# Kernel tuning notes

Measured on AMD Instinct MI355X. Metric: run time of the kernel, lower is better.

The kernel has to match this reference:

```python
import jax, jax.numpy as jnp
import numpy as np

LAT_SIZE = 2048
BATCH = 4096


def cos_pos_encoding_1d(size, freq_div=2.0, sub_freq_max=4.0):
    freqs = list(range(1, int(size / freq_div)))
    spaces = [np.linspace(0, freq * 2 * np.pi, size) for freq in freqs]
    sub_freqs = [1.0 / float(i) for i in range(2, int(sub_freq_max))]
    sub_spaces = [np.linspace(i * freq * 2 * np.pi, (i + 1) * freq * 2 * np.pi, size)
                  for freq in sub_freqs for i in range(int(1 / freq))]
    spaces = spaces + sub_spaces
    cos = [np.cos(space) for space in spaces]
    return np.stack(cos).astype(np.float32)  # (n_freq, size)


def setup_inputs() -> dict:
    key = jax.random.key(0)
    k1, k2 = jax.random.split(key)
    cos_basis = jnp.asarray(cos_pos_encoding_1d(LAT_SIZE, 1, 8))  # (2074, 2048)
    n_freq = cos_basis.shape[0]
    x = jax.random.normal(k1, (BATCH, LAT_SIZE), dtype=jnp.float32)
    # nn.Linear default init: U(-1/sqrt(in), 1/sqrt(in))
    bound = 1.0 / np.sqrt(LAT_SIZE)
    W = jax.random.uniform(k2, (n_freq, LAT_SIZE), dtype=jnp.float32,
                           minval=-bound, maxval=bound)
    return {"x": x, "W": W, "cos_basis": cos_basis}


def reference(x, W, cos_basis):
    # x: (B, lat), W: (n_freq, lat), cos_basis: (n_freq, lat)
    x_freqs = x @ W.T                          # (B, n_freq)  -- to_freq_size
    # broadcast-mul + sum over freq dim == GEMM against fixed cosine basis
    out = x_freqs @ cos_basis                  # (B, lat)
    # global max-normalize (norm=True)
    return out / jnp.max(out)
```

## Files before the change

### kernel.cpp

```cpp
#include <hip/hip_runtime.h>
#include <hip/hip_bf16.h>
#include <cstdint>

#define BATCH 4096
#define LAT   2048
#define NFREQ 2074
#define KPAD  2112

typedef __bf16 bf16x8 __attribute__((ext_vector_type(8)));
typedef float  f32x4  __attribute__((ext_vector_type(4)));

__device__ __forceinline__ unsigned short f2bf(float f) {
    unsigned int u = __float_as_uint(f);
    u = (u + 0x7fffu + ((u >> 16) & 1u)) >> 16;
    return (unsigned short)u;
}

__device__ __forceinline__ void gload_lds16(const unsigned short* g, unsigned short* l) {
    __builtin_amdgcn_global_load_lds(
        (const __attribute__((address_space(1))) unsigned int*)g,
        (__attribute__((address_space(3))) unsigned int*)l,
        16, 0, 0);
}


__global__ void prep_kernel(const float* __restrict__ W,
                            const float* __restrict__ cb,
                            unsigned short* __restrict__ WT,
                            unsigned short* __restrict__ cosT,
                            float* __restrict__ maxp) {
    __shared__ float t[64][65];
    const int bid = blockIdx.x;
    const int tid = threadIdx.x;
    if (bid == 0 && tid == 0) *maxp = -__builtin_inff();
    const float* in     = (bid < 1056) ? W  : cb;
    unsigned short* out = (bid < 1056) ? WT : cosT;
    int b2 = (bid < 1056) ? bid : bid - 1056;
    const int c0 = (b2 % 32) * 64;
    const int r0 = (b2 / 32) * 64;
    for (int i = tid; i < 1024; i += 256) {
        int rr = i >> 4;
        int c4 = (i & 15) * 4;
        int r  = r0 + rr;
        float4 v;
        if (r < NFREQ) v = *(const float4*)&in[(size_t)r * LAT + c0 + c4];
        else           v = make_float4(0.f, 0.f, 0.f, 0.f);
        t[rr][c4 + 0] = v.x; t[rr][c4 + 1] = v.y;
        t[rr][c4 + 2] = v.z; t[rr][c4 + 3] = v.w;
    }
    __syncthreads();
    for (int i = tid; i < 1024; i += 256) {
        int cc = i >> 4;
        int r4 = (i & 15) * 4;
        ushort4 o;
        o.x = f2bf(t[r4 + 0][cc]); o.y = f2bf(t[r4 + 1][cc]);
        o.z = f2bf(t[r4 + 2][cc]); o.w = f2bf(t[r4 + 3][cc]);
        *(ushort4*)&out[(size_t)(c0 + cc) * KPAD + r0 + r4] = o;
    }
}

template <int N, int K>
__global__ __launch_bounds__(512, 4)
void gemm1_kernel(const unsigned short* __restrict__ A,
                  const unsigned short* __restrict__ Bt,
                  unsigned short* __restrict__ C,
                  const float* __restrict__ x,
                  unsigned short* __restrict__ xb) {
    if (blockIdx.y >= 16) {
        const int cb  = (blockIdx.y - 16) * 16 + blockIdx.x;
        const int tid = threadIdx.x;
        const float4* x4 = (const float4*)x;
        uint4* o4 = (uint4*)xb;
        int i = cb * 512 + tid;
#pragma unroll
        for (int it = 0; it < 8; ++it, i += 131072) {
            float4 a = x4[2 * i];
            float4 b = x4[2 * i + 1];
            union { unsigned short us[8]; uint4 v; } p;
            p.us[0] = f2bf(a.x); p.us[1] = f2bf(a.y); p.us[2] = f2bf(a.z); p.us[3] = f2bf(a.w);
            p.us[4] = f2bf(b.x); p.us[5] = f2bf(b.y); p.us[6] = f2bf(b.z); p.us[7] = f2bf(b.w);
            o4[i] = p.v;
        }
        return;
    }

    __shared__ alignas(16) unsigned short As[3][128 * 32];
    __shared__ alignas(16) unsigned short Bs[3][128 * 32];

    const int tid  = threadIdx.x;
    const int wave = tid >> 6;
    const int lane = tid & 63;
    const int wm   = (wave >> 2) * 64;
    const int wn   = (wave & 3) * 32;
    const int quad = lane >> 4;
    const int l16  = lane & 15;

    const int mBase = blockIdx.y * 128;
    const int nBase = blockIdx.x * 128;

    const int srow = lane >> 2;
    const int sk   = (((lane & 3) ^ ((srow >> 1) & 3))) * 8;

    const unsigned short* Ab1 = A  + (size_t)(mBase + wave * 16 + srow) * K + sk;
    const unsigned short* Bb1 = Bt + (size_t)(nBase + wave * 16 + srow) * K + sk;
    const int coff = (wave * 16) * 32;

    const int pc = (quad ^ ((l16 >> 1) & 3)) * 8;

    constexpr int NIT = K / 32;
    gload_lds16(Ab1, &As[0][coff]);
    gload_lds16(Bb1, &Bs[0][coff]);

    f32x4 acc[4][2] = {};
    int bc = 0;
    for (int j = 0; j < NIT; ++j) {
        const int bn = (bc == 2) ? 0 : bc + 1;
        if (j + 1 < NIT) {
            const int k0 = (j + 1) * 32;
            gload_lds16(Ab1 + k0, &As[bn][coff]);
            gload_lds16(Bb1 + k0, &Bs[bn][coff]);
            asm volatile("s_waitcnt vmcnt(2)\n\ts_barrier" ::: "memory");
        } else {
            asm volatile("s_waitcnt vmcnt(0)\n\ts_barrier" ::: "memory");
        }
        bf16x8 af[4], bfr[2];
#pragma unroll
        for (int mi = 0; mi < 4; ++mi)
            af[mi] = *(const bf16x8*)&As[bc][(wm + mi * 16 + l16) * 32 + pc];
#pragma unroll
        for (int ni = 0; ni < 2; ++ni)
            bfr[ni] = *(const bf16x8*)&Bs[bc][(wn + ni * 16 + l16) * 32 + pc];
#pragma unroll
        for (int mi = 0; mi < 4; ++mi)
#pragma unroll
            for (int ni = 0; ni < 2; ++ni)
                acc[mi][ni] = __builtin_amdgcn_mfma_f32_16x16x32_bf16(
                    af[mi], bfr[ni], acc[mi][ni], 0, 0, 0);
        bc = bn;
    }

#pragma unroll
    for (int mi = 0; mi < 4; ++mi)
#pragma unroll
        for (int ni = 0; ni < 2; ++ni) {
            int col = nBase + wn + ni * 16 + l16;
#pragma unroll
            for (int r = 0; r < 4; ++r) {
                int row = mBase + wm + mi * 16 + quad * 4 + r;
                C[(size_t)row * N + col] = f2bf(acc[mi][ni][r]);
            }
        }
}

template <int N, int K>
__global__ __launch_bounds__(512, 4)
void gemm2_kernel(const unsigned short* __restrict__ A,
                  const unsigned short* __restrict__ Bt,
                  float* __restrict__ C,
                  float* __restrict__ maxp) {
    __shared__ alignas(16) unsigned short As[3][128 * 32];
    __shared__ alignas(16) unsigned short Bs[3][128 * 32];
    __shared__ float redbuf[8];

    const int tid  = threadIdx.x;
    const int wave = tid >> 6;
    const int lane = tid & 63;
    const int wm   = (wave >> 2) * 64;
    const int wn   = (wave & 3) * 32;
    const int quad = lane >> 4;
    const int l16  = lane & 15;

    const int mBase = blockIdx.y * 128;
    const int nBase = blockIdx.x * 128;

    const int srow = lane >> 2;
    const int sk   = (((lane & 3) ^ ((srow >> 1) & 3))) * 8;

    const unsigned short* Ab1 = A  + (size_t)(mBase + wave * 16 + srow) * K + sk;
    const unsigned short* Bb1 = Bt + (size_t)(nBase + wave * 16 + srow) * K + sk;
    const int coff = (wave * 16) * 32;

    const int pc = (quad ^ ((l16 >> 1) & 3)) * 8;

    constexpr int NIT = K / 32;
    gload_lds16(Ab1, &As[0][coff]);
    gload_lds16(Bb1, &Bs[0][coff]);

    f32x4 acc[4][2] = {};
    int bc = 0;
    for (int j = 0; j < NIT; ++j) {
        const int bn = (bc == 2) ? 0 : bc + 1;
        if (j + 1 < NIT) {
            const int k0 = (j + 1) * 32;
            gload_lds16(Ab1 + k0, &As[bn][coff]);
            gload_lds16(Bb1 + k0, &Bs[bn][coff]);
            asm volatile("s_waitcnt vmcnt(2)\n\ts_barrier" ::: "memory");
        } else {
            asm volatile("s_waitcnt vmcnt(0)\n\ts_barrier" ::: "memory");
        }
        bf16x8 af[4], bfr[2];
#pragma unroll
        for (int mi = 0; mi < 4; ++mi)
            af[mi] = *(const bf16x8*)&As[bc][(wm + mi * 16 + l16) * 32 + pc];
#pragma unroll
        for (int ni = 0; ni < 2; ++ni)
            bfr[ni] = *(const bf16x8*)&Bs[bc][(wn + ni * 16 + l16) * 32 + pc];
#pragma unroll
        for (int mi = 0; mi < 4; ++mi)
#pragma unroll
            for (int ni = 0; ni < 2; ++ni)
                acc[mi][ni] = __builtin_amdgcn_mfma_f32_16x16x32_bf16(
                    af[mi], bfr[ni], acc[mi][ni], 0, 0, 0);
        bc = bn;
    }

    float vmax = -__builtin_inff();
#pragma unroll
    for (int mi = 0; mi < 4; ++mi)
#pragma unroll
        for (int ni = 0; ni < 2; ++ni) {
            int col = nBase + wn + ni * 16 + l16;
#pragma unroll
            for (int r = 0; r < 4; ++r) {
                int row = mBase + wm + mi * 16 + quad * 4 + r;
                float v = acc[mi][ni][r];
                C[(size_t)row * N + col] = v;
                vmax = fmaxf(vmax, v);
            }
        }
#pragma unroll
    for (int off = 32; off > 0; off >>= 1)
        vmax = fmaxf(vmax, __shfl_xor(vmax, off));
    if (lane == 0) redbuf[wave] = vmax;
    __syncthreads();
    if (tid == 0) {
        float m = redbuf[0];
#pragma unroll
        for (int w = 1; w < 8; ++w) m = fmaxf(m, redbuf[w]);
        if (m >= 0.0f) atomicMax((int*)maxp, __float_as_int(m));
        else           atomicMin((unsigned int*)maxp, __float_as_uint(m));
    }
}

__global__ void scale_kernel(float* __restrict__ out, const float* __restrict__ maxp) {
    int i = blockIdx.x * blockDim.x + threadIdx.x;
    float inv = 1.0f / (*maxp);
    float4* o4 = (float4*)out;
    float4 v = o4[i];
    v.x *= inv; v.y *= inv; v.z *= inv; v.w *= inv;
    o4[i] = v;
}

extern "C" void kernel_launch(void* const* d_in, const int* in_sizes, int n_in,
                              void* d_out, int out_size, void* d_ws, size_t ws_size,
                              hipStream_t stream) {
    const float* x  = (const float*)d_in[0];
    const float* W  = (const float*)d_in[1];
    const float* cb = (const float*)d_in[2];

    char* ws = (char*)d_ws;
    unsigned short* xb   = (unsigned short*)ws;
    unsigned short* WT   = (unsigned short*)(ws + (size_t)BATCH * LAT * 2);
    unsigned short* cosT = (unsigned short*)((char*)WT + (size_t)LAT * KPAD * 2);
    unsigned short* C1   = (unsigned short*)((char*)cosT + (size_t)LAT * KPAD * 2);
    float*          maxp = (float*)((char*)C1 + (size_t)LAT * LAT * 2);
    float*          out  = (float*)d_out;

    prep_kernel<<<2 * 1056, 256, 0, stream>>>(W, cb, WT, cosT, maxp);

    gemm1_kernel<LAT, KPAD>
        <<<dim3(16, 32), 512, 0, stream>>>(cosT, WT, C1, x, xb);

    gemm2_kernel<LAT, LAT>
        <<<dim3(LAT / 128, BATCH / 128), 512, 0, stream>>>(xb, C1, out, maxp);

    scale_kernel<<<(out_size / 4) / 256, 256, 0, stream>>>(out, maxp);
}
```

Measured before the change: 191.6 us.

## Store GEMM2 output as bf16 intermediate and widen block to 1024 threads

GEMM2 now writes a bf16 intermediate through nontemporal stores instead of fp32 output, and the scale kernel reads that bf16 buffer and writes the final fp32 normalized result. This cuts the write-then-reread fp32 round trip between GEMM2 and the scale pass. The GEMM2 block goes to 1024 threads (16 waves), each wave holding a 32x32 tile and issuing one LDS load instead of two, to raise wave-level parallelism. GEMM1 output stores also become nontemporal. Rounding the output to bf16 before scaling adds precision loss, and the 1024-thread blocks with (1024,8) launch bounds may constrain registers.

```diff
diff --git a/kernel.cpp b/kernel.cpp
--- a/kernel.cpp
+++ b/kernel.cpp
@@ -147,25 +147,26 @@
 #pragma unroll
             for (int r = 0; r < 4; ++r) {
                 int row = mBase + wm + mi * 16 + quad * 4 + r;
-                C[(size_t)row * N + col] = f2bf(acc[mi][ni][r]);
+                __builtin_nontemporal_store(f2bf(acc[mi][ni][r]),
+                                            &C[(size_t)row * N + col]);
             }
         }
 }
 
 template <int N, int K>
-__global__ __launch_bounds__(512, 4)
+__global__ __launch_bounds__(1024, 8)
 void gemm2_kernel(const unsigned short* __restrict__ A,
                   const unsigned short* __restrict__ Bt,
-                  float* __restrict__ C,
+                  unsigned short* __restrict__ Cb,
                   float* __restrict__ maxp) {
     __shared__ alignas(16) unsigned short As[3][128 * 32];
     __shared__ alignas(16) unsigned short Bs[3][128 * 32];
-    __shared__ float redbuf[8];
+    __shared__ float redbuf[16];
 
     const int tid  = threadIdx.x;
     const int wave = tid >> 6;
     const int lane = tid & 63;
-    const int wm   = (wave >> 2) * 64;
+    const int wm   = (wave >> 2) * 32;
     const int wn   = (wave & 3) * 32;
     const int quad = lane >> 4;
     const int l16  = lane & 15;
@@ -176,37 +177,39 @@
     const int srow = lane >> 2;
     const int sk   = (((lane & 3) ^ ((srow >> 1) & 3))) * 8;
 
-    const unsigned short* Ab1 = A  + (size_t)(mBase + wave * 16 + srow) * K + sk;
-    const unsigned short* Bb1 = Bt + (size_t)(nBase + wave * 16 + srow) * K + sk;
-    const int coff = (wave * 16) * 32;
+    const int schunk = (wave & 7) * 16;
+    const unsigned short* Gb = (wave < 8)
+        ? A  + (size_t)(mBase + schunk + srow) * K + sk
+        : Bt + (size_t)(nBase + schunk + srow) * K + sk;
+    unsigned short* Lb0 = (wave < 8) ? &As[0][schunk * 32] : &Bs[0][schunk * 32];
+    unsigned short* Lb1 = (wave < 8) ? &As[1][schunk * 32] : &Bs[1][schunk * 32];
+    unsigned short* Lb2 = (wave < 8) ? &As[2][schunk * 32] : &Bs[2][schunk * 32];
+    unsigned short* Lbs[3] = {Lb0, Lb1, Lb2};
 
     const int pc = (quad ^ ((l16 >> 1) & 3)) * 8;
 
     constexpr int NIT = K / 32;
-    gload_lds16(Ab1, &As[0][coff]);
-    gload_lds16(Bb1, &Bs[0][coff]);
-
-    f32x4 acc[4][2] = {};
+    gload_lds16(Gb, Lbs[0]);
+
+    f32x4 acc[2][2] = {};
     int bc = 0;
     for (int j = 0; j < NIT; ++j) {
         const int bn = (bc == 2) ? 0 : bc + 1;
         if (j + 1 < NIT) {
-            const int k0 = (j + 1) * 32;
-            gload_lds16(Ab1 + k0, &As[bn][coff]);
-            gload_lds16(Bb1 + k0, &Bs[bn][coff]);
-            asm volatile("s_waitcnt vmcnt(2)\n\ts_barrier" ::: "memory");
+            gload_lds16(Gb + (j + 1) * 32, Lbs[bn]);
+            asm volatile("s_waitcnt vmcnt(1)\n\ts_barrier" ::: "memory");
         } else {
             asm volatile("s_waitcnt vmcnt(0)\n\ts_barrier" ::: "memory");
         }
-        bf16x8 af[4], bfr[2];
-#pragma unroll
-        for (int mi = 0; mi < 4; ++mi)
+        bf16x8 af[2], bfr[2];
+#pragma unroll
+        for (int mi = 0; mi < 2; ++mi)
             af[mi] = *(const bf16x8*)&As[bc][(wm + mi * 16 + l16) * 32 + pc];
 #pragma unroll
         for (int ni = 0; ni < 2; ++ni)
             bfr[ni] = *(const bf16x8*)&Bs[bc][(wn + ni * 16 + l16) * 32 + pc];
 #pragma unroll
-        for (int mi = 0; mi < 4; ++mi)
+        for (int mi = 0; mi < 2; ++mi)
 #pragma unroll
             for (int ni = 0; ni < 2; ++ni)
                 acc[mi][ni] = __builtin_amdgcn_mfma_f32_16x16x32_bf16(
@@ -216,7 +219,7 @@
 
     float vmax = -__builtin_inff();
 #pragma unroll
-    for (int mi = 0; mi < 4; ++mi)
+    for (int mi = 0; mi < 2; ++mi)
 #pragma unroll
         for (int ni = 0; ni < 2; ++ni) {
             int col = nBase + wn + ni * 16 + l16;
@@ -224,7 +227,7 @@
             for (int r = 0; r < 4; ++r) {
                 int row = mBase + wm + mi * 16 + quad * 4 + r;
                 float v = acc[mi][ni][r];
-                C[(size_t)row * N + col] = v;
+                __builtin_nontemporal_store(f2bf(v), &Cb[(size_t)row * N + col]);
                 vmax = fmaxf(vmax, v);
             }
         }
@@ -236,19 +239,30 @@
     if (tid == 0) {
         float m = redbuf[0];
 #pragma unroll
-        for (int w = 1; w < 8; ++w) m = fmaxf(m, redbuf[w]);
+        for (int w = 1; w < 16; ++w) m = fmaxf(m, redbuf[w]);
         if (m >= 0.0f) atomicMax((int*)maxp, __float_as_int(m));
         else           atomicMin((unsigned int*)maxp, __float_as_uint(m));
     }
 }
 
-__global__ void scale_kernel(float* __restrict__ out, const float* __restrict__ maxp) {
+__global__ void scale_kernel(const unsigned short* __restrict__ cb,
+                             float* __restrict__ out,
+                             const float* __restrict__ maxp) {
     int i = blockIdx.x * blockDim.x + threadIdx.x;
     float inv = 1.0f / (*maxp);
-    float4* o4 = (float4*)out;
-    float4 v = o4[i];
-    v.x *= inv; v.y *= inv; v.z *= inv; v.w *= inv;
-    o4[i] = v;
+    union { uint4 v; unsigned short us[8]; } p;
+    p.v = ((const uint4*)cb)[i];
+    float4 o0, o1;
+    o0.x = __uint_as_float((unsigned int)p.us[0] << 16) * inv;
+    o0.y = __uint_as_float((unsigned int)p.us[1] << 16) * inv;
+    o0.z = __uint_as_float((unsigned int)p.us[2] << 16) * inv;
+    o0.w = __uint_as_float((unsigned int)p.us[3] << 16) * inv;
+    o1.x = __uint_as_float((unsigned int)p.us[4] << 16) * inv;
+    o1.y = __uint_as_float((unsigned int)p.us[5] << 16) * inv;
+    o1.z = __uint_as_float((unsigned int)p.us[6] << 16) * inv;
+    o1.w = __uint_as_float((unsigned int)p.us[7] << 16) * inv;
+    ((float4*)out)[2 * i]     = o0;
+    ((float4*)out)[2 * i + 1] = o1;
 }
 
 extern "C" void kernel_launch(void* const* d_in, const int* in_sizes, int n_in,
@@ -263,7 +277,8 @@
     unsigned short* WT   = (unsigned short*)(ws + (size_t)BATCH * LAT * 2);
     unsigned short* cosT = (unsigned short*)((char*)WT + (size_t)LAT * KPAD * 2);
     unsigned short* C1   = (unsigned short*)((char*)cosT + (size_t)LAT * KPAD * 2);
-    float*          maxp = (float*)((char*)C1 + (size_t)LAT * LAT * 2);
+    unsigned short* C2b  = (unsigned short*)((char*)C1 + (size_t)LAT * LAT * 2);
+    float*          maxp = (float*)((char*)C2b + (size_t)BATCH * LAT * 2);
     float*          out  = (float*)d_out;
 
     prep_kernel<<<2 * 1056, 256, 0, stream>>>(W, cb, WT, cosT, maxp);
@@ -272,7 +287,7 @@
         <<<dim3(16, 32), 512, 0, stream>>>(cosT, WT, C1, x, xb);
 
     gemm2_kernel<LAT, LAT>
-        <<<dim3(LAT / 128, BATCH / 128), 512, 0, stream>>>(xb, C1, out, maxp);
-
-    scale_kernel<<<(out_size / 4) / 256, 256, 0, stream>>>(out, maxp);
-}
+        <<<dim3(LAT / 128, BATCH / 128), 1024, 0, stream>>>(xb, C1, C2b, maxp);
+
+    scale_kernel<<<(out_size / 8) / 256, 256, 0, stream>>>(C2b, out, maxp);
+}
```

New measurement: 198.1 us. 3.4% more time.

## Enlarge gemm2 block tile to 256x128 with BK=64 and 64x64 warp tiles

Applied to the files above, without the earlier changes.

The second GEMM now uses a 256x128 block tile with a K-step of 64, and each wave owns a 64x64 output tile (16 accumulators) instead of 64x32. LDS staging moves to 64-wide rows with an XOR swizzle over 8 chunks, and there are fewer barriers per unit of K. The aim is more MFMA work per LDS read and per sync, which raises arithmetic intensity. In exchange it uses more registers and LDS (launch bounds drop to 2 blocks per CU) and launches half as many blocks, which reduces occupancy.

```diff
diff --git a/kernel.cpp b/kernel.cpp
--- a/kernel.cpp
+++ b/kernel.cpp
@@ -153,64 +153,91 @@
 }
 
 template <int N, int K>
-__global__ __launch_bounds__(512, 4)
+__global__ __launch_bounds__(512, 2)
 void gemm2_kernel(const unsigned short* __restrict__ A,
                   const unsigned short* __restrict__ Bt,
                   float* __restrict__ C,
                   float* __restrict__ maxp) {
-    __shared__ alignas(16) unsigned short As[3][128 * 32];
-    __shared__ alignas(16) unsigned short Bs[3][128 * 32];
+    __shared__ alignas(16) unsigned short As[3][256 * 64];
+    __shared__ alignas(16) unsigned short Bs[3][128 * 64];
     __shared__ float redbuf[8];
 
     const int tid  = threadIdx.x;
     const int wave = tid >> 6;
     const int lane = tid & 63;
-    const int wm   = (wave >> 2) * 64;
-    const int wn   = (wave & 3) * 32;
+    const int wm   = (wave >> 1) * 64;
+    const int wn   = (wave & 1) * 64;
     const int quad = lane >> 4;
     const int l16  = lane & 15;
 
-    const int mBase = blockIdx.y * 128;
+    const int mBase = blockIdx.y * 256;
     const int nBase = blockIdx.x * 128;
 
-    const int srow = lane >> 2;
-    const int sk   = (((lane & 3) ^ ((srow >> 1) & 3))) * 8;
-
-    const unsigned short* Ab1 = A  + (size_t)(mBase + wave * 16 + srow) * K + sk;
-    const unsigned short* Bb1 = Bt + (size_t)(nBase + wave * 16 + srow) * K + sk;
-    const int coff = (wave * 16) * 32;
-
-    const int pc = (quad ^ ((l16 >> 1) & 3)) * 8;
-
-    constexpr int NIT = K / 32;
-    gload_lds16(Ab1, &As[0][coff]);
-    gload_lds16(Bb1, &Bs[0][coff]);
-
-    f32x4 acc[4][2] = {};
+    const int lrow = lane >> 3;
+    const int lchk = ((lane & 7) ^ lrow) * 8;
+    const unsigned short* Ab = A  + (size_t)(mBase + wave * 32 + lrow) * K + lchk;
+    const unsigned short* Bb = Bt + (size_t)(nBase + wave * 16 + lrow) * K + lchk;
+    const int aoff = (wave * 32) * 64;
+    const int boff = (wave * 16) * 64;
+
+    const int r7  = l16 & 7;
+    const int pc0 = ((0 * 4 + quad) ^ r7) * 8;
+    const int pc1 = ((1 * 4 + quad) ^ r7) * 8;
+
+    constexpr int NIT = K / 64;
+#pragma unroll
+    for (int d = 0; d < 4; ++d)
+        gload_lds16(Ab + (size_t)(d * 8) * K, &As[0][aoff + d * 8 * 64]);
+#pragma unroll
+    for (int d = 0; d < 2; ++d)
+        gload_lds16(Bb + (size_t)(d * 8) * K, &Bs[0][boff + d * 8 * 64]);
+
+    f32x4 acc[4][4] = {};
     int bc = 0;
     for (int j = 0; j < NIT; ++j) {
         const int bn = (bc == 2) ? 0 : bc + 1;
         if (j + 1 < NIT) {
-            const int k0 = (j + 1) * 32;
-            gload_lds16(Ab1 + k0, &As[bn][coff]);
-            gload_lds16(Bb1 + k0, &Bs[bn][coff]);
-            asm volatile("s_waitcnt vmcnt(2)\n\ts_barrier" ::: "memory");
+            const int k0 = (j + 1) * 64;
+#pragma unroll
+            for (int d = 0; d < 4; ++d)
+                gload_lds16(Ab + (size_t)(d * 8) * K + k0, &As[bn][aoff + d * 8 * 64]);
+#pragma unroll
+            for (int d = 0; d < 2; ++d)
+                gload_lds16(Bb + (size_t)(d * 8) * K + k0, &Bs[bn][boff + d * 8 * 64]);
+            asm volatile("s_waitcnt vmcnt(6)\n\ts_barrier" ::: "memory");
         } else {
             asm volatile("s_waitcnt vmcnt(0)\n\ts_barrier" ::: "memory");
         }
-        bf16x8 af[4], bfr[2];
-#pragma unroll
-        for (int mi = 0; mi < 4; ++mi)
-            af[mi] = *(const bf16x8*)&As[bc][(wm + mi * 16 + l16) * 32 + pc];
-#pragma unroll
-        for (int ni = 0; ni < 2; ++ni)
-            bfr[ni] = *(const bf16x8*)&Bs[bc][(wn + ni * 16 + l16) * 32 + pc];
-#pragma unroll
-        for (int mi = 0; mi < 4; ++mi)
-#pragma unroll
-            for (int ni = 0; ni < 2; ++ni)
-                acc[mi][ni] = __builtin_amdgcn_mfma_f32_16x16x32_bf16(
-                    af[mi], bfr[ni], acc[mi][ni], 0, 0, 0);
+        {
+            bf16x8 af[4], bfr[4];
+#pragma unroll
+            for (int mi = 0; mi < 4; ++mi)
+                af[mi] = *(const bf16x8*)&As[bc][(wm + mi * 16 + l16) * 64 + pc0];
+#pragma unroll
+            for (int ni = 0; ni < 4; ++ni)
+                bfr[ni] = *(const bf16x8*)&Bs[bc][(wn + ni * 16 + l16) * 64 + pc0];
+#pragma unroll
+            for (int mi = 0; mi < 4; ++mi)
+#pragma unroll
+                for (int ni = 0; ni < 4; ++ni)
+                    acc[mi][ni] = __builtin_amdgcn_mfma_f32_16x16x32_bf16(
+                        af[mi], bfr[ni], acc[mi][ni], 0, 0, 0);
+        }
+        {
+            bf16x8 af[4], bfr[4];
+#pragma unroll
+            for (int mi = 0; mi < 4; ++mi)
+                af[mi] = *(const bf16x8*)&As[bc][(wm + mi * 16 + l16) * 64 + pc1];
+#pragma unroll
+            for (int ni = 0; ni < 4; ++ni)
+                bfr[ni] = *(const bf16x8*)&Bs[bc][(wn + ni * 16 + l16) * 64 + pc1];
+#pragma unroll
+            for (int mi = 0; mi < 4; ++mi)
+#pragma unroll
+                for (int ni = 0; ni < 4; ++ni)
+                    acc[mi][ni] = __builtin_amdgcn_mfma_f32_16x16x32_bf16(
+                        af[mi], bfr[ni], acc[mi][ni], 0, 0, 0);
+        }
         bc = bn;
     }
 
@@ -218,7 +245,7 @@
 #pragma unroll
     for (int mi = 0; mi < 4; ++mi)
 #pragma unroll
-        for (int ni = 0; ni < 2; ++ni) {
+        for (int ni = 0; ni < 4; ++ni) {
             int col = nBase + wn + ni * 16 + l16;
 #pragma unroll
             for (int r = 0; r < 4; ++r) {
@@ -272,7 +299,7 @@
         <<<dim3(16, 32), 512, 0, stream>>>(cosT, WT, C1, x, xb);
 
     gemm2_kernel<LAT, LAT>
-        <<<dim3(LAT / 128, BATCH / 128), 512, 0, stream>>>(xb, C1, out, maxp);
+        <<<dim3(LAT / 128, BATCH / 256), 512, 0, stream>>>(xb, C1, out, maxp);
 
     scale_kernel<<<(out_size / 4) / 256, 256, 0, stream>>>(out, maxp);
 }
```

Result: faster. 181.7 us (-5.2%).
